# Performance work log

Measured on AMD Instinct MI355X. Metric: run time of the kernel, lower is better.

## Reference

```python
import jax, jax.numpy as jnp
import numpy as np

K1 = 3                      # spline kernel size per pseudo dim
SIZE = float(np.sqrt(2.0))  # pseudo_cartesian normalization size


def spline_weights(p, k):
    """Degree-1 open B-spline basis over 2D pseudo coords.
    p: [..., 2] in [0,1]. Returns basis [..., 4], weight_index [..., 4]."""
    v = jnp.clip(p, 0.0, 1.0) * (k - 1)
    lo = jnp.floor(v)
    frac = v - lo
    lo = lo.astype(jnp.int32)
    off = jnp.array([0, 1], dtype=jnp.int32)
    w0 = jnp.stack([1.0 - frac[..., 0], frac[..., 0]], axis=-1)   # [...,2]
    w1 = jnp.stack([1.0 - frac[..., 1], frac[..., 1]], axis=-1)   # [...,2]
    i0 = jnp.clip(lo[..., 0:1] + off, 0, k - 1)                    # [...,2]
    i1 = jnp.clip(lo[..., 1:2] + off, 0, k - 1)                    # [...,2]
    basis = (w0[..., :, None] * w1[..., None, :]).reshape(*p.shape[:-1], 4)
    widx = (i0[..., :, None] + k * i1[..., None, :]).reshape(*p.shape[:-1], 4)
    return basis, widx


def setup_inputs() -> dict:
    key = jax.random.key(0)
    kx, ke, kp, kq, kw, kb = jax.random.split(key, 6)
    N, C, P, E, K = 50000, 64, 16, 800000, K1 * K1
    x = jax.random.normal(kx, (N, C), dtype=jnp.float32)
    pos = jax.random.uniform(kp, (N, 2), dtype=jnp.float32)
    pose = jax.random.normal(kq, (N, P, 2), dtype=jnp.float32)
    pose = pose / (jnp.linalg.norm(pose, axis=-1, keepdims=True) + 1e-8)  # unit pose vectors
    W = jax.random.normal(kw, (P, K, C), dtype=jnp.float32) / np.sqrt(C * 4.0)
    bias = jax.random.normal(kb, (P,), dtype=jnp.float32) * 0.01
    edge_index = jax.random.randint(ke, (2, E), 0, N, dtype=jnp.int64)
    return {"x": x, "pos": pos, "pose": pose, "W": W, "bias": bias,
            "edge_index": edge_index}


def reference(x, pos, pose, W, bias, edge_index):
    N, C = x.shape
    P = pose.shape[1]
    row, col = edge_index[0], edge_index[1]
    # pseudo_cartesian: normalized relative position in [0,1]^2
    pseudo = (pos[col] - pos[row]) / (2.0 * SIZE) + 0.5              # [E,2]
    # posevec_to_rotmat on detached pose vectors
    pose_c = jax.lax.stop_gradient(pose)
    a, b = pose_c[..., 0], pose_c[..., 1]
    R = jnp.stack([jnp.stack([a, -b], -1), jnp.stack([b, a], -1)], -2)  # [N,P,2,2]
    Re = R[row]                                                      # [E,P,2,2]
    # rotate pseudo coords about (0.5, 0.5), batched over all poses
    p = jnp.einsum('epij,ej->epi', Re, pseudo - 0.5) + 0.5           # [E,P,2]
    basis, widx = spline_weights(p, K1)                              # [E,P,4]
    # SplineConv (out_channels=1, no root weight, no norm):
    # precompute per-node per-pose per-kernel-bin projections
    Z = jnp.einsum('nc,pkc->npk', x, W)                              # [N,P,K]
    pidx = jnp.arange(P)[None, :, None]
    vals = Z[col[:, None, None], pidx, widx]                         # [E,P,4]
    msg = jnp.sum(basis * vals, axis=-1)                             # [E,P]
    out = jax.ops.segment_sum(msg, row, num_segments=N)              # [N,P]
    return out + bias[None, :]
```

## Files before the change

kernel.cpp:

```cpp
#include <hip/hip_runtime.h>

#define C_DIM 64
#define P_DIM 16
#define K_DIM 9
#define ZROW 10
#define ZNODE (P_DIM * ZROW)
#define NT 10
#define INV2S 0.35355339059327373f

typedef __attribute__((ext_vector_type(8))) short short8v;
typedef __attribute__((ext_vector_type(4))) float f32x4;
typedef uint uint4a __attribute__((ext_vector_type(4), aligned(4)));

__device__ __forceinline__ ushort f2bf(float f) {
    uint u = __builtin_bit_cast(uint, f);
    return (ushort)((u + 0x7FFFu + ((u >> 16) & 1u)) >> 16);
}
__device__ __forceinline__ float bf2f(ushort h) {
    return __builtin_bit_cast(float, ((uint)h) << 16);
}

#define WSTRIDE 72

__global__ __launch_bounds__(256) void z_gemm_kernel(const float* __restrict__ x,
                                                     const float* __restrict__ W,
                                                     const float* __restrict__ bias,
                                                     const float* __restrict__ pose,
                                                     float* __restrict__ out,
                                                     ushort* __restrict__ Zb,
                                                     uint* __restrict__ pose_bf,
                                                     int N) {
    __shared__ ushort w_hi[160 * WSTRIDE];
    __shared__ ushort w_lo[160 * WSTRIDE];

    const int tid = threadIdx.x;
    const int block_row = blockIdx.x * 64;

    {
        const float4 b4 = ((const float4*)bias)[tid & 3];
        const int o4 = block_row * 4 + tid;
        if (o4 < N * 4) ((float4*)out)[o4] = b4;
    }

    if (pose_bf != nullptr) {
        for (int i = tid; i < 64 * P_DIM; i += 256) {
            const int r = block_row + (i >> 4);
            if (r < N) {
                const float2 ab = ((const float2*)pose)[(size_t)r * P_DIM + (i & 15)];
                pose_bf[(size_t)r * P_DIM + (i & 15)] =
                    (uint)f2bf(ab.x) | ((uint)f2bf(ab.y) << 16);
            }
        }
    }

    for (int i = tid; i < 160 * (C_DIM / 2); i += 256) {
        const int s  = i >> 5;
        const int k2 = i & 31;
        const int p  = s / 10;
        const int k  = s - p * 10;
        float2 w2 = make_float2(0.0f, 0.0f);
        if (k < 9) w2 = ((const float2*)W)[(p * 9 + k) * (C_DIM / 2) + k2];
        const int o = s * WSTRIDE + k2 * 2;
        const ushort h0 = f2bf(w2.x);
        const ushort h1 = f2bf(w2.y);
        w_hi[o]     = h0;
        w_hi[o + 1] = h1;
        w_lo[o]     = f2bf(w2.x - bf2f(h0));
        w_lo[o + 1] = f2bf(w2.y - bf2f(h1));
    }
    __syncthreads();

    const int lane = tid & 63;
    const int wv   = tid >> 6;
    const int col  = lane & 15;
    const int kg   = lane >> 4;

    const int arow = block_row + wv * 16 + col;
    const float* xr = x + (size_t)(arow < N ? arow : 0) * C_DIM;
    float4 x0 = ((const float4*)xr)[kg * 2];
    float4 x1 = ((const float4*)xr)[kg * 2 + 1];
    float4 x2 = ((const float4*)xr)[8 + kg * 2];
    float4 x3 = ((const float4*)xr)[8 + kg * 2 + 1];
    if (arow >= N) {
        x0 = x1 = x2 = x3 = make_float4(0.f, 0.f, 0.f, 0.f);
    }

    short8v a_hi0, a_lo0, a_hi1, a_lo1;
    {
        const float t0[8] = {x0.x, x0.y, x0.z, x0.w, x1.x, x1.y, x1.z, x1.w};
        const float t1[8] = {x2.x, x2.y, x2.z, x2.w, x3.x, x3.y, x3.z, x3.w};
        #pragma unroll
        for (int e = 0; e < 8; ++e) {
            const ushort h = f2bf(t0[e]);
            a_hi0[e] = (short)h;
            a_lo0[e] = (short)f2bf(t0[e] - bf2f(h));
            const ushort g = f2bf(t1[e]);
            a_hi1[e] = (short)g;
            a_lo1[e] = (short)f2bf(t1[e] - bf2f(g));
        }
    }

    const int orow0 = block_row + wv * 16 + kg * 4;

    #pragma unroll
    for (int nt = 0; nt < NT; ++nt) {
        const int j = nt * 16 + col;
        const ushort* bhp = &w_hi[j * WSTRIDE + kg * 8];
        const ushort* blp = &w_lo[j * WSTRIDE + kg * 8];
        const short8v bh0 = *(const short8v*)bhp;
        const short8v bh1 = *(const short8v*)(bhp + 32);
        const short8v bl0 = *(const short8v*)blp;
        const short8v bl1 = *(const short8v*)(blp + 32);

        f32x4 acc = {0.f, 0.f, 0.f, 0.f};
        acc = __builtin_amdgcn_mfma_f32_16x16x32_bf16(a_lo0, bh0, acc, 0, 0, 0);
        acc = __builtin_amdgcn_mfma_f32_16x16x32_bf16(a_hi0, bl0, acc, 0, 0, 0);
        acc = __builtin_amdgcn_mfma_f32_16x16x32_bf16(a_lo1, bh1, acc, 0, 0, 0);
        acc = __builtin_amdgcn_mfma_f32_16x16x32_bf16(a_hi1, bl1, acc, 0, 0, 0);
        acc = __builtin_amdgcn_mfma_f32_16x16x32_bf16(a_hi0, bh0, acc, 0, 0, 0);
        acc = __builtin_amdgcn_mfma_f32_16x16x32_bf16(a_hi1, bh1, acc, 0, 0, 0);

        #pragma unroll
        for (int r = 0; r < 4; ++r) {
            const int row = orow0 + r;
            if (row < N) Zb[(size_t)row * ZNODE + j] = f2bf(acc[r]);
        }
    }
}

#define EILP 8
template <bool USEBF>
__global__ __launch_bounds__(256) void edge_kernel(const int* __restrict__ ei,
                                                   const float* __restrict__ pos,
                                                   const float* __restrict__ pose,
                                                   const uint* __restrict__ pose_bf,
                                                   const ushort* __restrict__ Zb,
                                                   float* __restrict__ out,
                                                   int E, int ebase, int eend) {
    const int p  = threadIdx.x & 15;
    const int eg = threadIdx.x >> 4;
    const int e0 = ebase + blockIdx.x * (16 * EILP) + eg;

    int  r[EILP], c[EILP];
    bool valid[EILP];
    #pragma unroll
    for (int it = 0; it < EILP; ++it) {
        int e = e0 + it * 16;
        valid[it] = (e < eend);
        int ec = valid[it] ? e : 0;
        r[it] = ei[ec];
        c[it] = ei[E + ec];
    }

    float d0[EILP], d1[EILP];
    #pragma unroll
    for (int it = 0; it < EILP; ++it) {
        const float2 pc = ((const float2*)pos)[c[it]];
        const float2 pr = ((const float2*)pos)[r[it]];
        d0[it] = (pc.x - pr.x) * INV2S;
        d1[it] = (pc.y - pr.y) * INV2S;
    }

    float a_[EILP], b_[EILP];
    #pragma unroll
    for (int it = 0; it < EILP; ++it) {
        if (USEBF) {
            const uint ab = pose_bf[(size_t)r[it] * P_DIM + p];
            a_[it] = bf2f((ushort)(ab & 0xffffu));
            b_[it] = bf2f((ushort)(ab >> 16));
        } else {
            const float2 ab = ((const float2*)pose)[(size_t)r[it] * P_DIM + p];
            a_[it] = ab.x;
            b_[it] = ab.y;
        }
    }

    uint4a qv[EILP];
    uint   q4[EILP];
    #pragma unroll
    for (int it = 0; it < EILP; ++it) {
        const uint* Zp = (const uint*)(Zb + (size_t)c[it] * ZNODE) + p * (ZROW / 2);
        qv[it] = *(const uint4a*)Zp;
        q4[it] = Zp[4];
    }

    #pragma unroll
    for (int it = 0; it < EILP; ++it) {
        const float p0 = fmaf(a_[it], d0[it], fmaf(-b_[it], d1[it], 0.5f));
        const float p1 = fmaf(b_[it], d0[it], fmaf( a_[it], d1[it], 0.5f));

        const float v0 = fminf(fmaxf(p0, 0.0f), 1.0f) * 2.0f;
        const float v1 = fminf(fmaxf(p1, 0.0f), 1.0f) * 2.0f;
        const bool b0 = (v0 >= 1.0f);
        const bool b1 = (v1 >= 1.0f);
        const float f0 = v0 - (b0 ? 1.0f : 0.0f);
        const float f1 = v1 - (b1 ? 1.0f : 0.0f);

        const uint A0 = qv[it][0], A1 = qv[it][1], A2 = qv[it][2],
                   A3 = qv[it][3], A4 = q4[it];
        const uint W0 = b1 ? ((A1 >> 16) | (A2 << 16)) : A0;
        const uint W1 = b1 ? ((A2 >> 16) | (A3 << 16)) : A1;
        const uint W2 = b1 ? ((A3 >> 16) | (A4 << 16)) : A2;
        const uint s = b0 ? 16u : 0u;
        const float z00 = bf2f((ushort)(W0 >> s));
        const float z10 = bf2f((ushort)(b0 ? (W1 & 0xffffu) : (W0 >> 16)));
        const float z01 = bf2f((ushort)(b0 ? (W2 & 0xffffu) : (W1 >> 16)));
        const float z11 = bf2f((ushort)(W2 >> s));

        const float w00 = (1.0f - f0) * (1.0f - f1);
        const float w01 = (1.0f - f0) * f1;
        const float w10 = f0 * (1.0f - f1);
        const float w11 = f0 * f1;

        float m = w00 * z00;
        m = fmaf(w01, z01, m);
        m = fmaf(w10, z10, m);
        m = fmaf(w11, z11, m);

        if (valid[it]) atomicAdd(&out[(size_t)r[it] * P_DIM + p], m);
    }
}

extern "C" void kernel_launch(void* const* d_in, const int* in_sizes, int n_in,
                              void* d_out, int out_size, void* d_ws, size_t ws_size,
                              hipStream_t stream) {
    const float* x    = (const float*)d_in[0];
    const float* pos  = (const float*)d_in[1];
    const float* pose = (const float*)d_in[2];
    const float* W    = (const float*)d_in[3];
    const float* bias = (const float*)d_in[4];
    const int*   ei   = (const int*)d_in[5];

    const int N = in_sizes[0] / C_DIM;
    const int E = in_sizes[5] / 2;

    float* out = (float*)d_out;
    ushort* Zb = (ushort*)d_ws;

    const size_t zb_bytes   = (size_t)N * ZNODE * sizeof(ushort);
    const size_t pose_bytes = (size_t)N * P_DIM * sizeof(uint);
    uint* pose_bf = (ws_size >= zb_bytes + pose_bytes)
                        ? (uint*)((char*)d_ws + zb_bytes) : nullptr;

    z_gemm_kernel<<<(N + 63) / 64, 256, 0, stream>>>(x, W, bias, pose, out, Zb, pose_bf, N);

    const int Eh  = E / 2;
    const int eb1 = (Eh + 16 * EILP - 1) / (16 * EILP);
    const int eb2 = ((E - Eh) + 16 * EILP - 1) / (16 * EILP);
    if (pose_bf != nullptr) {
        edge_kernel<true><<<eb1, 256, 0, stream>>>(ei, pos, pose, pose_bf, Zb, out, E, 0, Eh);
        edge_kernel<true><<<eb2, 256, 0, stream>>>(ei, pos, pose, pose_bf, Zb, out, E, Eh, E);
    } else {
        edge_kernel<false><<<eb1, 256, 0, stream>>>(ei, pos, pose, pose_bf, Zb, out, E, 0, Eh);
        edge_kernel<false><<<eb2, 256, 0, stream>>>(ei, pos, pose, pose_bf, Zb, out, E, Eh, E);
    }
}
```

Measured before the change: 158.5 us.

## Process 256 rows per GEMM block and merge edge kernel launches

The Z GEMM kernel now has each wave handle four 16-row M tiles, so 256 rows per block instead of 64. The bf16 hi/lo conversion of W into shared memory is amortised over four times as many rows, and the B fragments loaded from LDS are reused across the four tiles. The two half-range edge kernel launches are collapsed into a single launch over all edges, removing one launch and its tail. The cost is more registers per thread for the A fragments and four times fewer GEMM blocks (about 196), which may underfill the GPU.

```diff
diff --git a/kernel.cpp b/kernel.cpp
--- a/kernel.cpp
+++ b/kernel.cpp
@@ -6,6 +6,7 @@
 #define ZROW 10
 #define ZNODE (P_DIM * ZROW)
 #define NT 10
+#define BROWS 256
 #define INV2S 0.35355339059327373f
 
 typedef __attribute__((ext_vector_type(8))) short short8v;
@@ -34,16 +35,19 @@
     __shared__ ushort w_lo[160 * WSTRIDE];
 
     const int tid = threadIdx.x;
-    const int block_row = blockIdx.x * 64;
+    const int block_row = blockIdx.x * BROWS;
 
     {
         const float4 b4 = ((const float4*)bias)[tid & 3];
-        const int o4 = block_row * 4 + tid;
-        if (o4 < N * 4) ((float4*)out)[o4] = b4;
+        #pragma unroll
+        for (int i = tid; i < BROWS * 4; i += 256) {
+            const int row = block_row + (i >> 2);
+            if (row < N) ((float4*)out)[(size_t)row * 4 + (i & 3)] = b4;
+        }
     }
 
     if (pose_bf != nullptr) {
-        for (int i = tid; i < 64 * P_DIM; i += 256) {
+        for (int i = tid; i < BROWS * P_DIM; i += 256) {
             const int r = block_row + (i >> 4);
             if (r < N) {
                 const float2 ab = ((const float2*)pose)[(size_t)r * P_DIM + (i & 15)];
@@ -75,32 +79,30 @@
     const int col  = lane & 15;
     const int kg   = lane >> 4;
 
-    const int arow = block_row + wv * 16 + col;
-    const float* xr = x + (size_t)(arow < N ? arow : 0) * C_DIM;
-    float4 x0 = ((const float4*)xr)[kg * 2];
-    float4 x1 = ((const float4*)xr)[kg * 2 + 1];
-    float4 x2 = ((const float4*)xr)[8 + kg * 2];
-    float4 x3 = ((const float4*)xr)[8 + kg * 2 + 1];
-    if (arow >= N) {
-        x0 = x1 = x2 = x3 = make_float4(0.f, 0.f, 0.f, 0.f);
-    }
-
-    short8v a_hi0, a_lo0, a_hi1, a_lo1;
-    {
+    short8v ah[4][2], al[4][2];
+    #pragma unroll
+    for (int mt = 0; mt < 4; ++mt) {
+        const int arow = block_row + wv * 64 + mt * 16 + col;
+        const float* xr = x + (size_t)(arow < N ? arow : 0) * C_DIM;
+        float4 x0 = ((const float4*)xr)[kg * 2];
+        float4 x1 = ((const float4*)xr)[kg * 2 + 1];
+        float4 x2 = ((const float4*)xr)[8 + kg * 2];
+        float4 x3 = ((const float4*)xr)[8 + kg * 2 + 1];
+        if (arow >= N) {
+            x0 = x1 = x2 = x3 = make_float4(0.f, 0.f, 0.f, 0.f);
+        }
         const float t0[8] = {x0.x, x0.y, x0.z, x0.w, x1.x, x1.y, x1.z, x1.w};
         const float t1[8] = {x2.x, x2.y, x2.z, x2.w, x3.x, x3.y, x3.z, x3.w};
         #pragma unroll
         for (int e = 0; e < 8; ++e) {
             const ushort h = f2bf(t0[e]);
-            a_hi0[e] = (short)h;
-            a_lo0[e] = (short)f2bf(t0[e] - bf2f(h));
+            ah[mt][0][e] = (short)h;
+            al[mt][0][e] = (short)f2bf(t0[e] - bf2f(h));
             const ushort g = f2bf(t1[e]);
-            a_hi1[e] = (short)g;
-            a_lo1[e] = (short)f2bf(t1[e] - bf2f(g));
-        }
-    }
-
-    const int orow0 = block_row + wv * 16 + kg * 4;
+            ah[mt][1][e] = (short)g;
+            al[mt][1][e] = (short)f2bf(t1[e] - bf2f(g));
+        }
+    }
 
     #pragma unroll
     for (int nt = 0; nt < NT; ++nt) {
@@ -112,18 +114,22 @@
         const short8v bl0 = *(const short8v*)blp;
         const short8v bl1 = *(const short8v*)(blp + 32);
 
-        f32x4 acc = {0.f, 0.f, 0.f, 0.f};
-        acc = __builtin_amdgcn_mfma_f32_16x16x32_bf16(a_lo0, bh0, acc, 0, 0, 0);
-        acc = __builtin_amdgcn_mfma_f32_16x16x32_bf16(a_hi0, bl0, acc, 0, 0, 0);
-        acc = __builtin_amdgcn_mfma_f32_16x16x32_bf16(a_lo1, bh1, acc, 0, 0, 0);
-        acc = __builtin_amdgcn_mfma_f32_16x16x32_bf16(a_hi1, bl1, acc, 0, 0, 0);
-        acc = __builtin_amdgcn_mfma_f32_16x16x32_bf16(a_hi0, bh0, acc, 0, 0, 0);
-        acc = __builtin_amdgcn_mfma_f32_16x16x32_bf16(a_hi1, bh1, acc, 0, 0, 0);
-
         #pragma unroll
-        for (int r = 0; r < 4; ++r) {
-            const int row = orow0 + r;
-            if (row < N) Zb[(size_t)row * ZNODE + j] = f2bf(acc[r]);
+        for (int mt = 0; mt < 4; ++mt) {
+            f32x4 acc = {0.f, 0.f, 0.f, 0.f};
+            acc = __builtin_amdgcn_mfma_f32_16x16x32_bf16(al[mt][0], bh0, acc, 0, 0, 0);
+            acc = __builtin_amdgcn_mfma_f32_16x16x32_bf16(ah[mt][0], bl0, acc, 0, 0, 0);
+            acc = __builtin_amdgcn_mfma_f32_16x16x32_bf16(al[mt][1], bh1, acc, 0, 0, 0);
+            acc = __builtin_amdgcn_mfma_f32_16x16x32_bf16(ah[mt][1], bl1, acc, 0, 0, 0);
+            acc = __builtin_amdgcn_mfma_f32_16x16x32_bf16(ah[mt][0], bh0, acc, 0, 0, 0);
+            acc = __builtin_amdgcn_mfma_f32_16x16x32_bf16(ah[mt][1], bh1, acc, 0, 0, 0);
+
+            const int orow0 = block_row + wv * 64 + mt * 16 + kg * 4;
+            #pragma unroll
+            for (int r = 0; r < 4; ++r) {
+                const int row = orow0 + r;
+                if (row < N) Zb[(size_t)row * ZNODE + j] = f2bf(acc[r]);
+            }
         }
     }
 }
@@ -136,17 +142,17 @@
                                                    const uint* __restrict__ pose_bf,
                                                    const ushort* __restrict__ Zb,
                                                    float* __restrict__ out,
-                                                   int E, int ebase, int eend) {
+                                                   int E) {
     const int p  = threadIdx.x & 15;
     const int eg = threadIdx.x >> 4;
-    const int e0 = ebase + blockIdx.x * (16 * EILP) + eg;
+    const int e0 = blockIdx.x * (16 * EILP) + eg;
 
     int  r[EILP], c[EILP];
     bool valid[EILP];
     #pragma unroll
     for (int it = 0; it < EILP; ++it) {
         int e = e0 + it * 16;
-        valid[it] = (e < eend);
+        valid[it] = (e < E);
         int ec = valid[it] ? e : 0;
         r[it] = ei[ec];
         c[it] = ei[E + ec];
@@ -242,16 +248,11 @@
     uint* pose_bf = (ws_size >= zb_bytes + pose_bytes)
                         ? (uint*)((char*)d_ws + zb_bytes) : nullptr;
 
-    z_gemm_kernel<<<(N + 63) / 64, 256, 0, stream>>>(x, W, bias, pose, out, Zb, pose_bf, N);
-
-    const int Eh  = E / 2;
-    const int eb1 = (Eh + 16 * EILP - 1) / (16 * EILP);
-    const int eb2 = ((E - Eh) + 16 * EILP - 1) / (16 * EILP);
-    if (pose_bf != nullptr) {
-        edge_kernel<true><<<eb1, 256, 0, stream>>>(ei, pos, pose, pose_bf, Zb, out, E, 0, Eh);
-        edge_kernel<true><<<eb2, 256, 0, stream>>>(ei, pos, pose, pose_bf, Zb, out, E, Eh, E);
-    } else {
-        edge_kernel<false><<<eb1, 256, 0, stream>>>(ei, pos, pose, pose_bf, Zb, out, E, 0, Eh);
-        edge_kernel<false><<<eb2, 256, 0, stream>>>(ei, pos, pose, pose_bf, Zb, out, E, Eh, E);
-    }
-}
+    z_gemm_kernel<<<(N + BROWS - 1) / BROWS, 256, 0, stream>>>(x, W, bias, pose, out, Zb, pose_bf, N);
+
+    const int eblocks = (E + 16 * EILP - 1) / (16 * EILP);
+    if (pose_bf != nullptr)
+        edge_kernel<true><<<eblocks, 256, 0, stream>>>(ei, pos, pose, pose_bf, Zb, out, E);
+    else
+        edge_kernel<false><<<eblocks, 256, 0, stream>>>(ei, pos, pose, pose_bf, Zb, out, E);
+}
```

Measured after the change: 153.9 us. 1.03x faster.

## Partition edges by source-node range across blocks for cache locality of Z gathers

Applied to the files above, without the earlier changes.

The edge kernel now has 8 blocks per edge chunk group, each handling only the edges whose column node falls in one eighth of the node range. Edges are compacted with a ballot and shuffles, four edges per wave pass. The aim is to keep the Z rows and pose gathers of each block within a smaller working set so they hit better in L2 and Infinity Cache. In exchange, every block reads each edge index eight times, adds ballot and shuffle overhead, and waves run partly empty where the compacted counts don't fill four slots.

```diff
diff --git a/kernel.cpp b/kernel.cpp
--- a/kernel.cpp
+++ b/kernel.cpp
@@ -128,7 +128,6 @@
     }
 }
 
-#define EILP 8
 template <bool USEBF>
 __global__ __launch_bounds__(256) void edge_kernel(const int* __restrict__ ei,
                                                    const float* __restrict__ pos,
@@ -136,88 +135,97 @@
                                                    const uint* __restrict__ pose_bf,
                                                    const ushort* __restrict__ Zb,
                                                    float* __restrict__ out,
-                                                   int E, int ebase, int eend) {
-    const int p  = threadIdx.x & 15;
-    const int eg = threadIdx.x >> 4;
-    const int e0 = ebase + blockIdx.x * (16 * EILP) + eg;
-
-    int  r[EILP], c[EILP];
-    bool valid[EILP];
+                                                   int E, float invn8) {
+    const int wid  = threadIdx.x >> 6;
+    const int lane = threadIdx.x & 63;
+    const int p    = lane & 15;
+    const int g    = lane >> 4;
+    const int sub  = blockIdx.x & 7;
+    const int cg0  = (blockIdx.x >> 3) * 16 + wid * 4;
+
     #pragma unroll
-    for (int it = 0; it < EILP; ++it) {
-        int e = e0 + it * 16;
-        valid[it] = (e < eend);
-        int ec = valid[it] ? e : 0;
-        r[it] = ei[ec];
-        c[it] = ei[E + ec];
-    }
-
-    float d0[EILP], d1[EILP];
-    #pragma unroll
-    for (int it = 0; it < EILP; ++it) {
-        const float2 pc = ((const float2*)pos)[c[it]];
-        const float2 pr = ((const float2*)pos)[r[it]];
-        d0[it] = (pc.x - pr.x) * INV2S;
-        d1[it] = (pc.y - pr.y) * INV2S;
-    }
-
-    float a_[EILP], b_[EILP];
-    #pragma unroll
-    for (int it = 0; it < EILP; ++it) {
-        if (USEBF) {
-            const uint ab = pose_bf[(size_t)r[it] * P_DIM + p];
-            a_[it] = bf2f((ushort)(ab & 0xffffu));
-            b_[it] = bf2f((ushort)(ab >> 16));
-        } else {
-            const float2 ab = ((const float2*)pose)[(size_t)r[it] * P_DIM + p];
-            a_[it] = ab.x;
-            b_[it] = ab.y;
-        }
-    }
-
-    uint4a qv[EILP];
-    uint   q4[EILP];
-    #pragma unroll
-    for (int it = 0; it < EILP; ++it) {
-        const uint* Zp = (const uint*)(Zb + (size_t)c[it] * ZNODE) + p * (ZROW / 2);
-        qv[it] = *(const uint4a*)Zp;
-        q4[it] = Zp[4];
-    }
-
-    #pragma unroll
-    for (int it = 0; it < EILP; ++it) {
-        const float p0 = fmaf(a_[it], d0[it], fmaf(-b_[it], d1[it], 0.5f));
-        const float p1 = fmaf(b_[it], d0[it], fmaf( a_[it], d1[it], 0.5f));
-
-        const float v0 = fminf(fmaxf(p0, 0.0f), 1.0f) * 2.0f;
-        const float v1 = fminf(fmaxf(p1, 0.0f), 1.0f) * 2.0f;
-        const bool b0 = (v0 >= 1.0f);
-        const bool b1 = (v1 >= 1.0f);
-        const float f0 = v0 - (b0 ? 1.0f : 0.0f);
-        const float f1 = v1 - (b1 ? 1.0f : 0.0f);
-
-        const uint A0 = qv[it][0], A1 = qv[it][1], A2 = qv[it][2],
-                   A3 = qv[it][3], A4 = q4[it];
-        const uint W0 = b1 ? ((A1 >> 16) | (A2 << 16)) : A0;
-        const uint W1 = b1 ? ((A2 >> 16) | (A3 << 16)) : A1;
-        const uint W2 = b1 ? ((A3 >> 16) | (A4 << 16)) : A2;
-        const uint s = b0 ? 16u : 0u;
-        const float z00 = bf2f((ushort)(W0 >> s));
-        const float z10 = bf2f((ushort)(b0 ? (W1 & 0xffffu) : (W0 >> 16)));
-        const float z01 = bf2f((ushort)(b0 ? (W2 & 0xffffu) : (W1 >> 16)));
-        const float z11 = bf2f((ushort)(W2 >> s));
-
-        const float w00 = (1.0f - f0) * (1.0f - f1);
-        const float w01 = (1.0f - f0) * f1;
-        const float w10 = f0 * (1.0f - f1);
-        const float w11 = f0 * f1;
-
-        float m = w00 * z00;
-        m = fmaf(w01, z01, m);
-        m = fmaf(w10, z10, m);
-        m = fmaf(w11, z11, m);
-
-        if (valid[it]) atomicAdd(&out[(size_t)r[it] * P_DIM + p], m);
+    for (int it = 0; it < 4; ++it) {
+        const int chunk = cg0 + it;
+        const int e  = chunk * 64 + lane;
+        const bool ev = (e < E);
+        const int ee = ev ? e : 0;
+        const int cl = __builtin_nontemporal_load(ei + (size_t)E + ee);
+        const int rl = __builtin_nontemporal_load(ei + ee);
+        const int subc = (int)((float)cl * invn8);
+        const bool inr = ev && (subc == sub);
+
+        unsigned long long mask = __ballot(inr);
+        while (mask) {
+            uint packed = 0;
+            int nv = 0;
+            #pragma unroll
+            for (int t = 0; t < 4; ++t) {
+                if (mask) {
+                    const uint li = (uint)__builtin_ctzll(mask);
+                    mask &= (mask - 1);
+                    packed |= li << (8 * t);
+                    ++nv;
+                }
+            }
+            const uint Lg = (packed >> ((lane >> 1) & 24)) & 63u;
+            const bool gv = (g < nv);
+            int rg = __shfl(rl, (int)Lg, 64);
+            int cg = __shfl(cl, (int)Lg, 64);
+            rg = gv ? rg : 0;
+            cg = gv ? cg : 0;
+
+            const float2 pc = ((const float2*)pos)[cg];
+            const float2 pr = ((const float2*)pos)[rg];
+            const float d0 = (pc.x - pr.x) * INV2S;
+            const float d1 = (pc.y - pr.y) * INV2S;
+
+            float a_, b_;
+            if (USEBF) {
+                const uint ab = pose_bf[(size_t)rg * P_DIM + p];
+                a_ = bf2f((ushort)(ab & 0xffffu));
+                b_ = bf2f((ushort)(ab >> 16));
+            } else {
+                const float2 ab = ((const float2*)pose)[(size_t)rg * P_DIM + p];
+                a_ = ab.x;
+                b_ = ab.y;
+            }
+
+            const uint* Zp = (const uint*)(Zb + (size_t)cg * ZNODE) + p * (ZROW / 2);
+            const uint4a qv = *(const uint4a*)Zp;
+            const uint   q4 = Zp[4];
+
+            const float p0 = fmaf(a_, d0, fmaf(-b_, d1, 0.5f));
+            const float p1 = fmaf(b_, d0, fmaf( a_, d1, 0.5f));
+
+            const float v0 = fminf(fmaxf(p0, 0.0f), 1.0f) * 2.0f;
+            const float v1 = fminf(fmaxf(p1, 0.0f), 1.0f) * 2.0f;
+            const bool b0 = (v0 >= 1.0f);
+            const bool b1 = (v1 >= 1.0f);
+            const float f0 = v0 - (b0 ? 1.0f : 0.0f);
+            const float f1 = v1 - (b1 ? 1.0f : 0.0f);
+
+            const uint A0 = qv[0], A1 = qv[1], A2 = qv[2], A3 = qv[3], A4 = q4;
+            const uint W0 = b1 ? ((A1 >> 16) | (A2 << 16)) : A0;
+            const uint W1 = b1 ? ((A2 >> 16) | (A3 << 16)) : A1;
+            const uint W2 = b1 ? ((A3 >> 16) | (A4 << 16)) : A2;
+            const uint s = b0 ? 16u : 0u;
+            const float z00 = bf2f((ushort)(W0 >> s));
+            const float z10 = bf2f((ushort)(b0 ? (W1 & 0xffffu) : (W0 >> 16)));
+            const float z01 = bf2f((ushort)(b0 ? (W2 & 0xffffu) : (W1 >> 16)));
+            const float z11 = bf2f((ushort)(W2 >> s));
+
+            const float w00 = (1.0f - f0) * (1.0f - f1);
+            const float w01 = (1.0f - f0) * f1;
+            const float w10 = f0 * (1.0f - f1);
+            const float w11 = f0 * f1;
+
+            float msg = w00 * z00;
+            msg = fmaf(w01, z01, msg);
+            msg = fmaf(w10, z10, msg);
+            msg = fmaf(w11, z11, msg);
+
+            if (gv) atomicAdd(&out[(size_t)rg * P_DIM + p], msg);
+        }
     }
 }
 
@@ -244,14 +252,11 @@
 
     z_gemm_kernel<<<(N + 63) / 64, 256, 0, stream>>>(x, W, bias, pose, out, Zb, pose_bf, N);
 
-    const int Eh  = E / 2;
-    const int eb1 = (Eh + 16 * EILP - 1) / (16 * EILP);
-    const int eb2 = ((E - Eh) + 16 * EILP - 1) / (16 * EILP);
-    if (pose_bf != nullptr) {
-        edge_kernel<true><<<eb1, 256, 0, stream>>>(ei, pos, pose, pose_bf, Zb, out, E, 0, Eh);
-        edge_kernel<true><<<eb2, 256, 0, stream>>>(ei, pos, pose, pose_bf, Zb, out, E, Eh, E);
-    } else {
-        edge_kernel<false><<<eb1, 256, 0, stream>>>(ei, pos, pose, pose_bf, Zb, out, E, 0, Eh);
-        edge_kernel<false><<<eb2, 256, 0, stream>>>(ei, pos, pose, pose_bf, Zb, out, E, Eh, E);
-    }
-}
+    const int NC = (E + 63) / 64;
+    const int cgroups = (NC + 15) / 16;
+    const float invn8 = 1.0f / (float)((N + 7) / 8);
+    if (pose_bf != nullptr)
+        edge_kernel<true><<<cgroups * 8, 256, 0, stream>>>(ei, pos, pose, pose_bf, Zb, out, E, invn8);
+    else
+        edge_kernel<false><<<cgroups * 8, 256, 0, stream>>>(ei, pos, pose, pose_bf, Zb, out, E, invn8);
+}
```

Result: slower. 174.0 us (+9.8%).
